# Kernel tuning notes

Hardware: AMD Instinct MI355X
Metric: run time of the kernel (lower is better)

## Reference

```python
import jax, jax.numpy as jnp
import numpy as np


def setup_inputs() -> dict:
    key = jax.random.key(0)
    k1, k2 = jax.random.split(key)
    B, N, C = 128, 200000, 100
    values = jax.random.normal(k1, (B, N), dtype=jnp.float32)
    labels = jax.random.randint(k2, (N,), 0, C, dtype=jnp.int64)
    return {"values": values, "labels": labels, "num_classes": C}


def reference(values, labels, num_classes):
    # Stratified (label-grouped) max pooling:
    # values: [B, N], labels: [N] in [0, num_classes)
    # output: [B, num_classes], out[b, c] = max over columns j with labels[j] == c
    # segment_max reduces over the leading axis, so operate on values.T [N, B].
    pooled = jax.ops.segment_max(
        values.T, labels, num_segments=num_classes, indices_are_sorted=False
    )  # [C, B]
    return pooled.T  # [B, C]
```

## Files before the change

kernel.cpp:

```cpp
#include <hip/hip_runtime.h>
#include <hip/hip_bf16.h>


#define TPB   256
#define ROWS  8
#define CACC  128

#define ENC_NEG_INF 0x007FFFFFu

__device__ __forceinline__ unsigned enc(float f) {
    unsigned u = __float_as_uint(f);
    return (u & 0x80000000u) ? ~u : (u | 0x80000000u);
}
__device__ __forceinline__ float dec(unsigned u) {
    unsigned b = (u & 0x80000000u) ? (u & 0x7FFFFFFFu) : ~u;
    return __uint_as_float(b);
}


__global__ __launch_bounds__(TPB) void strat_part(
    const float* __restrict__ values, const int* __restrict__ labels,
    unsigned* __restrict__ part, int B, int N, int C, int S, int T) {
    __shared__ unsigned acc[ROWS * CACC];

    const int tid  = threadIdx.x;
    const int bx   = blockIdx.x;
    const int row0 = blockIdx.y * ROWS;
    const int rmax = min(ROWS, B - row0);

    for (int i = tid; i < ROWS * CACC; i += TPB) acc[i] = ENC_NEG_INF;
    __syncthreads();

    for (int t = bx; t < T; t += S) {
        const int base = t * 1024 + tid * 4;
        if (t * 1024 + 1024 <= N) {
            const int4 L = *(const int4*)(labels + base);
            if (rmax == ROWS) {
                float4 v[ROWS];
#pragma unroll
                for (int r = 0; r < ROWS; ++r)
                    v[r] = *(const float4*)(values + (size_t)(row0 + r) * N + base);
#pragma unroll
                for (int r = 0; r < ROWS; ++r) {
                    unsigned* a = acc + r * CACC;
                    atomicMax(&a[L.x], enc(v[r].x));
                    atomicMax(&a[L.y], enc(v[r].y));
                    atomicMax(&a[L.z], enc(v[r].z));
                    atomicMax(&a[L.w], enc(v[r].w));
                }
            } else {
                for (int r = 0; r < rmax; ++r) {
                    float4 v = *(const float4*)(values + (size_t)(row0 + r) * N + base);
                    unsigned* a = acc + r * CACC;
                    atomicMax(&a[L.x], enc(v.x));
                    atomicMax(&a[L.y], enc(v.y));
                    atomicMax(&a[L.z], enc(v.z));
                    atomicMax(&a[L.w], enc(v.w));
                }
            }
        } else {
#pragma unroll
            for (int e = 0; e < 4; ++e) {
                const int j = base + e;
                if (j < N) {
                    const int c = labels[j];
                    for (int r = 0; r < rmax; ++r)
                        atomicMax(&acc[r * CACC + c],
                                  enc(values[(size_t)(row0 + r) * N + j]));
                }
            }
        }
    }

    __syncthreads();

    unsigned* dst = part + (size_t)bx * B * C;
    for (int i = tid; i < rmax * C; i += TPB) {
        const int r = i / C, c = i - r * C;
        dst[(size_t)(row0 + r) * C + c] = acc[r * CACC + c];
    }
}

__global__ __launch_bounds__(TPB) void strat_reduce(
    const unsigned* __restrict__ part, float* __restrict__ out, int BC, int S) {
    const int i = blockIdx.x * TPB + threadIdx.x;
    if (i >= BC) return;
    unsigned m = ENC_NEG_INF;
    for (int s = 0; s < S; ++s) m = max(m, part[(size_t)s * BC + i]);
    out[i] = dec(m);
}


#define FCPAD 257

__global__ __launch_bounds__(TPB) void strat_init(unsigned* __restrict__ out_enc, int n) {
    int i = blockIdx.x * TPB + threadIdx.x;
    if (i < n) out_enc[i] = ENC_NEG_INF;
}

__global__ __launch_bounds__(TPB) void strat_main_atomic(
    const float* __restrict__ values, const int* __restrict__ labels,
    unsigned* __restrict__ out_enc, int B, int N, int C, int T) {
    __shared__ unsigned acc[ROWS * FCPAD];
    const int tid  = threadIdx.x;
    const int row0 = blockIdx.y * ROWS;
    const int rmax = min(ROWS, B - row0);

    for (int i = tid; i < ROWS * FCPAD; i += TPB) acc[i] = ENC_NEG_INF;
    __syncthreads();

    const int t = blockIdx.x;
#pragma unroll
    for (int e = 0; e < 4; ++e) {
        const int j = t * 1024 + tid * 4 + e;
        if (j < N) {
            const int c = labels[j];
            for (int r = 0; r < rmax; ++r)
                atomicMax(&acc[r * FCPAD + c],
                          enc(values[(size_t)(row0 + r) * N + j]));
        }
    }
    __syncthreads();
    for (int i = tid; i < rmax * C; i += TPB) {
        const int r = i / C, c = i - r * C;
        atomicMax(&out_enc[(size_t)(row0 + r) * C + c], acc[r * FCPAD + c]);
    }
}

__global__ __launch_bounds__(TPB) void strat_decode(unsigned* __restrict__ buf, int n) {
    int i = blockIdx.x * TPB + threadIdx.x;
    if (i < n) {
        float f = dec(buf[i]);
        ((float*)buf)[i] = f;
    }
}


extern "C" void kernel_launch(void* const* d_in, const int* in_sizes, int n_in,
                              void* d_out, int out_size, void* d_ws, size_t ws_size,
                              hipStream_t stream) {
    const float* values = (const float*)d_in[0];
    const int*   labels = (const int*)d_in[1];
    const int N  = in_sizes[1];
    const int B  = in_sizes[0] / N;
    const int C  = out_size / B;
    const int BC = B * C;
    const int T  = (N + 1023) / 1024;
    const int RG = (B + ROWS - 1) / ROWS;

    int S = 98;
    const size_t per_split = (size_t)BC * sizeof(unsigned);
    if (per_split > 0 && (size_t)S * per_split > ws_size)
        S = (int)(ws_size / per_split);
    if (S > T) S = T;

    const bool main_ok = (S >= 1) && (C <= CACC) && (N % 4 == 0);

    if (main_ok) {
        unsigned* part = (unsigned*)d_ws;
        dim3 grid(S, RG);
        strat_part<<<grid, TPB, 0, stream>>>(values, labels, part, B, N, C, S, T);
        strat_reduce<<<(BC + TPB - 1) / TPB, TPB, 0, stream>>>(
            part, (float*)d_out, BC, S);
    } else {
        unsigned* out_enc = (unsigned*)d_out;
        const int init_blocks = (out_size + TPB - 1) / TPB;
        strat_init<<<init_blocks, TPB, 0, stream>>>(out_enc, out_size);
        dim3 grid(T, RG);
        strat_main_atomic<<<grid, TPB, 0, stream>>>(values, labels, out_enc, B, N, C, T);
        strat_decode<<<init_blocks, TPB, 0, stream>>>(out_enc, out_size);
    }
}
```

Baseline: 176.6 us.

## Replace LDS atomic max with single-wave transposed tiles and lane-per-row accumulators

The partial kernel now runs one 64-lane wave per block. Each wave stages a 64-column by 64-row tile in shared memory, and each lane owns one batch row, so per-class max updates become plain read-modify-write with no atomics or float encoding. The class label is broadcast with readlane. The reduction works directly on float partials laid out per row group and split. The tile is filled with strided column loads (each lane reads down a column of rows), which are poorly coalesced compared with the earlier float4 row loads. The accumulator takes 32KB of shared memory per block, which may limit occupancy.

```diff
diff --git a/kernel.cpp b/kernel.cpp
--- a/kernel.cpp
+++ b/kernel.cpp
@@ -2,10 +2,86 @@
 #include <hip/hip_bf16.h>
 
 
+#define WTPB 64
+#define JT   64
+#define TPAD 65
+#define CCAP 128
+#define NEGINF (-__builtin_huge_valf())
+
+__global__ __launch_bounds__(WTPB) void strat_tpose(
+    const float* __restrict__ values, const int* __restrict__ labels,
+    float* __restrict__ part, int B, int N, int C, int S, int T) {
+    __shared__ float tile[JT * TPAD];
+    __shared__ float acc[CCAP * WTPB];
+
+    const int lane = threadIdx.x;
+    const int s    = blockIdx.x;
+    const int rg   = blockIdx.y;
+    const int row0 = rg * WTPB;
+    const int rmax = min(WTPB, B - row0);
+
+    for (int i = lane; i < C * WTPB; i += WTPB) acc[i] = NEGINF;
+
+    for (int t = s; t < T; t += S) {
+        const int jc = t * JT + lane;
+        int lab = 0;
+        if (jc < N) lab = labels[jc];
+        const float* colp = values + (size_t)row0 * N + jc;
+        float* tcol = tile + lane * TPAD;
+
+        if (jc < N && rmax == WTPB) {
+#pragma unroll
+            for (int r = 0; r < WTPB; ++r)
+                tcol[r] = colp[(size_t)r * N];
+        } else {
+            for (int r = 0; r < WTPB; ++r)
+                tcol[r] = (jc < N && r < rmax) ? colp[(size_t)r * N] : NEGINF;
+        }
+
+#pragma unroll
+        for (int j = 0; j < JT; ++j) {
+            const int   c = __builtin_amdgcn_readlane(lab, j);
+            const float v = tile[j * TPAD + lane];
+            float* a = acc + c * WTPB + lane;
+            const float o = *a;
+            *a = fmaxf(o, v);
+        }
+    }
+
+    float* dst = part + ((size_t)rg * S + s) * ((size_t)C * WTPB);
+    for (int i = lane; i < C * WTPB; i += WTPB) dst[i] = acc[i];
+}
+
+__global__ __launch_bounds__(256) void strat_reduce2(
+    const float* __restrict__ part, float* __restrict__ out,
+    int B, int C, int S, int RG) {
+    const int PC = C * WTPB;
+    const int i  = blockIdx.x * 256 + threadIdx.x;
+    if (i >= RG * PC) return;
+    const int rg  = i / PC;
+    const int rem = i - rg * PC;
+    const int c   = rem >> 6;
+    const int l   = rem & 63;
+    const int b   = rg * WTPB + l;
+    if (b >= B) return;
+
+    const float* p = part + (size_t)rg * S * PC + rem;
+    float m0 = NEGINF, m1 = NEGINF, m2 = NEGINF, m3 = NEGINF;
+    int s = 0;
+    for (; s + 4 <= S; s += 4) {
+        m0 = fmaxf(m0, p[(size_t)(s + 0) * PC]);
+        m1 = fmaxf(m1, p[(size_t)(s + 1) * PC]);
+        m2 = fmaxf(m2, p[(size_t)(s + 2) * PC]);
+        m3 = fmaxf(m3, p[(size_t)(s + 3) * PC]);
+    }
+    for (; s < S; ++s) m0 = fmaxf(m0, p[(size_t)s * PC]);
+    out[b * C + c] = fmaxf(fmaxf(m0, m1), fmaxf(m2, m3));
+}
+
+
 #define TPB   256
 #define ROWS  8
-#define CACC  128
-
+#define FCPAD 257
 #define ENC_NEG_INF 0x007FFFFFu
 
 __device__ __forceinline__ unsigned enc(float f) {
@@ -16,82 +92,6 @@
     unsigned b = (u & 0x80000000u) ? (u & 0x7FFFFFFFu) : ~u;
     return __uint_as_float(b);
 }
-
-
-__global__ __launch_bounds__(TPB) void strat_part(
-    const float* __restrict__ values, const int* __restrict__ labels,
-    unsigned* __restrict__ part, int B, int N, int C, int S, int T) {
-    __shared__ unsigned acc[ROWS * CACC];
-
-    const int tid  = threadIdx.x;
-    const int bx   = blockIdx.x;
-    const int row0 = blockIdx.y * ROWS;
-    const int rmax = min(ROWS, B - row0);
-
-    for (int i = tid; i < ROWS * CACC; i += TPB) acc[i] = ENC_NEG_INF;
-    __syncthreads();
-
-    for (int t = bx; t < T; t += S) {
-        const int base = t * 1024 + tid * 4;
-        if (t * 1024 + 1024 <= N) {
-            const int4 L = *(const int4*)(labels + base);
-            if (rmax == ROWS) {
-                float4 v[ROWS];
-#pragma unroll
-                for (int r = 0; r < ROWS; ++r)
-                    v[r] = *(const float4*)(values + (size_t)(row0 + r) * N + base);
-#pragma unroll
-                for (int r = 0; r < ROWS; ++r) {
-                    unsigned* a = acc + r * CACC;
-                    atomicMax(&a[L.x], enc(v[r].x));
-                    atomicMax(&a[L.y], enc(v[r].y));
-                    atomicMax(&a[L.z], enc(v[r].z));
-                    atomicMax(&a[L.w], enc(v[r].w));
-                }
-            } else {
-                for (int r = 0; r < rmax; ++r) {
-                    float4 v = *(const float4*)(values + (size_t)(row0 + r) * N + base);
-                    unsigned* a = acc + r * CACC;
-                    atomicMax(&a[L.x], enc(v.x));
-                    atomicMax(&a[L.y], enc(v.y));
-                    atomicMax(&a[L.z], enc(v.z));
-                    atomicMax(&a[L.w], enc(v.w));
-                }
-            }
-        } else {
-#pragma unroll
-            for (int e = 0; e < 4; ++e) {
-                const int j = base + e;
-                if (j < N) {
-                    const int c = labels[j];
-                    for (int r = 0; r < rmax; ++r)
-                        atomicMax(&acc[r * CACC + c],
-                                  enc(values[(size_t)(row0 + r) * N + j]));
-                }
-            }
-        }
-    }
-
-    __syncthreads();
-
-    unsigned* dst = part + (size_t)bx * B * C;
-    for (int i = tid; i < rmax * C; i += TPB) {
-        const int r = i / C, c = i - r * C;
-        dst[(size_t)(row0 + r) * C + c] = acc[r * CACC + c];
-    }
-}
-
-__global__ __launch_bounds__(TPB) void strat_reduce(
-    const unsigned* __restrict__ part, float* __restrict__ out, int BC, int S) {
-    const int i = blockIdx.x * TPB + threadIdx.x;
-    if (i >= BC) return;
-    unsigned m = ENC_NEG_INF;
-    for (int s = 0; s < S; ++s) m = max(m, part[(size_t)s * BC + i]);
-    out[i] = dec(m);
-}
-
-
-#define FCPAD 257
 
 __global__ __launch_bounds__(TPB) void strat_init(unsigned* __restrict__ out_enc, int n) {
     int i = blockIdx.x * TPB + threadIdx.x;
@@ -144,30 +144,34 @@
     const int N  = in_sizes[1];
     const int B  = in_sizes[0] / N;
     const int C  = out_size / B;
-    const int BC = B * C;
-    const int T  = (N + 1023) / 1024;
-    const int RG = (B + ROWS - 1) / ROWS;
+    const int T  = (N + JT - 1) / JT;
+    const int RG = (B + WTPB - 1) / WTPB;
 
-    int S = 98;
-    const size_t per_split = (size_t)BC * sizeof(unsigned);
-    if (per_split > 0 && (size_t)S * per_split > ws_size)
-        S = (int)(ws_size / per_split);
+    int S = 768 / (RG > 0 ? RG : 1);
+    if (S < 1) S = 1;
     if (S > T) S = T;
+    size_t need = (size_t)RG * S * C * WTPB * sizeof(float);
+    while (S > 1 && need > ws_size) {
+        S >>= 1;
+        need = (size_t)RG * S * C * WTPB * sizeof(float);
+    }
 
-    const bool main_ok = (S >= 1) && (C <= CACC) && (N % 4 == 0);
+    const bool main_ok = (C <= CCAP) && (need <= ws_size) && (S >= 1);
 
     if (main_ok) {
-        unsigned* part = (unsigned*)d_ws;
+        float* part = (float*)d_ws;
         dim3 grid(S, RG);
-        strat_part<<<grid, TPB, 0, stream>>>(values, labels, part, B, N, C, S, T);
-        strat_reduce<<<(BC + TPB - 1) / TPB, TPB, 0, stream>>>(
-            part, (float*)d_out, BC, S);
+        strat_tpose<<<grid, WTPB, 0, stream>>>(values, labels, part, B, N, C, S, T);
+        const int outs = RG * C * WTPB;
+        strat_reduce2<<<(outs + 255) / 256, 256, 0, stream>>>(
+            part, (float*)d_out, B, C, S, RG);
     } else {
         unsigned* out_enc = (unsigned*)d_out;
         const int init_blocks = (out_size + TPB - 1) / TPB;
         strat_init<<<init_blocks, TPB, 0, stream>>>(out_enc, out_size);
-        dim3 grid(T, RG);
-        strat_main_atomic<<<grid, TPB, 0, stream>>>(values, labels, out_enc, B, N, C, T);
+        dim3 grid((N + 1023) / 1024, (B + ROWS - 1) / ROWS);
+        strat_main_atomic<<<grid, TPB, 0, stream>>>(values, labels, out_enc, B, N, C,
+                                                    (N + 1023) / 1024);
         strat_decode<<<init_blocks, TPB, 0, stream>>>(out_enc, out_size);
     }
 }
```

After: 201.3 us. +14.0%, slower.

## Restructure segment max into per-row span streaming with byte labels

Applied to the files above, without the earlier changes.

Labels are first compacted to 8-bit in the workspace. The main kernel then assigns each block a single row and a contiguous span of columns (16 spans per row), streams values with nontemporal vector loads, and spreads atomics over four padded LDS copies, one per group of 16 lanes within each wavefront, to cut contention. The final reduction loop is unrolled by four, and a branchless float encoding replaces the conditional one. The extra label-conversion launch and the loss of label reuse across eight rows trade against better load coalescing and fewer LDS conflicts.

```diff
diff --git a/kernel.cpp b/kernel.cpp
--- a/kernel.cpp
+++ b/kernel.cpp
@@ -2,96 +2,95 @@
 #include <hip/hip_bf16.h>
 
 
-#define TPB   256
-#define ROWS  8
-#define CACC  128
-
+#define TPBS 256
+#define SMAX 16
 #define ENC_NEG_INF 0x007FFFFFu
 
-__device__ __forceinline__ unsigned enc(float f) {
-    unsigned u = __float_as_uint(f);
-    return (u & 0x80000000u) ? ~u : (u | 0x80000000u);
+typedef float f4 __attribute__((ext_vector_type(4)));
+
+__device__ __forceinline__ unsigned enc32(unsigned u) {
+    return u ^ ((unsigned)(((int)u) >> 31) | 0x80000000u);
 }
-__device__ __forceinline__ float dec(unsigned u) {
-    unsigned b = (u & 0x80000000u) ? (u & 0x7FFFFFFFu) : ~u;
+__device__ __forceinline__ float dec32(unsigned u) {
+    unsigned b = u ^ (~(unsigned)(((int)u) >> 31) | 0x80000000u);
     return __uint_as_float(b);
 }
 
+__global__ __launch_bounds__(TPBS) void strat_lab8(
+    const int* __restrict__ labels, unsigned char* __restrict__ l8, int N) {
+    int i = blockIdx.x * TPBS + threadIdx.x;
+    if (i < N) l8[i] = (unsigned char)labels[i];
+}
 
-__global__ __launch_bounds__(TPB) void strat_part(
-    const float* __restrict__ values, const int* __restrict__ labels,
-    unsigned* __restrict__ part, int B, int N, int C, int S, int T) {
-    __shared__ unsigned acc[ROWS * CACC];
+__global__ __launch_bounds__(TPBS) void strat_stream(
+    const float* __restrict__ values, const unsigned char* __restrict__ l8,
+    unsigned* __restrict__ part, int B, int N, int C, int S, int SPAN, int CPAD) {
+    extern __shared__ unsigned acc[];
 
-    const int tid  = threadIdx.x;
-    const int bx   = blockIdx.x;
-    const int row0 = blockIdx.y * ROWS;
-    const int rmax = min(ROWS, B - row0);
+    const int tid = threadIdx.x;
+    const int blk = blockIdx.x;
+    const int s   = blk % S;
+    const int b   = blk / S;
 
-    for (int i = tid; i < ROWS * CACC; i += TPB) acc[i] = ENC_NEG_INF;
+    for (int i = tid; i < 4 * CPAD; i += TPBS) acc[i] = ENC_NEG_INF;
     __syncthreads();
 
-    for (int t = bx; t < T; t += S) {
-        const int base = t * 1024 + tid * 4;
-        if (t * 1024 + 1024 <= N) {
-            const int4 L = *(const int4*)(labels + base);
-            if (rmax == ROWS) {
-                float4 v[ROWS];
-#pragma unroll
-                for (int r = 0; r < ROWS; ++r)
-                    v[r] = *(const float4*)(values + (size_t)(row0 + r) * N + base);
-#pragma unroll
-                for (int r = 0; r < ROWS; ++r) {
-                    unsigned* a = acc + r * CACC;
-                    atomicMax(&a[L.x], enc(v[r].x));
-                    atomicMax(&a[L.y], enc(v[r].y));
-                    atomicMax(&a[L.z], enc(v[r].z));
-                    atomicMax(&a[L.w], enc(v[r].w));
-                }
-            } else {
-                for (int r = 0; r < rmax; ++r) {
-                    float4 v = *(const float4*)(values + (size_t)(row0 + r) * N + base);
-                    unsigned* a = acc + r * CACC;
-                    atomicMax(&a[L.x], enc(v.x));
-                    atomicMax(&a[L.y], enc(v.y));
-                    atomicMax(&a[L.z], enc(v.z));
-                    atomicMax(&a[L.w], enc(v.w));
-                }
-            }
-        } else {
-#pragma unroll
-            for (int e = 0; e < 4; ++e) {
-                const int j = base + e;
-                if (j < N) {
-                    const int c = labels[j];
-                    for (int r = 0; r < rmax; ++r)
-                        atomicMax(&acc[r * CACC + c],
-                                  enc(values[(size_t)(row0 + r) * N + j]));
-                }
-            }
+    const int off0 = s * SPAN;
+    const int len  = min(SPAN, N - off0);
+    if (len > 0) {
+        unsigned* qacc = acc + ((tid & 63) >> 4) * CPAD;
+        const f4* vp = (const f4*)(values + (size_t)b * N + off0);
+        const uchar4* lp = (const uchar4*)(l8 + off0);
+        const int nv = len >> 2;
+
+        for (int i = tid; i < nv; i += TPBS) {
+            f4 v = __builtin_nontemporal_load(vp + i);
+            uchar4 L = lp[i];
+            atomicMax(&qacc[L.x], enc32(__float_as_uint(v.x)));
+            atomicMax(&qacc[L.y], enc32(__float_as_uint(v.y)));
+            atomicMax(&qacc[L.z], enc32(__float_as_uint(v.z)));
+            atomicMax(&qacc[L.w], enc32(__float_as_uint(v.w)));
+        }
+        for (int i = (nv << 2) + tid; i < len; i += TPBS) {
+            atomicMax(&qacc[l8[off0 + i]],
+                      enc32(__float_as_uint(values[(size_t)b * N + off0 + i])));
         }
     }
-
     __syncthreads();
 
-    unsigned* dst = part + (size_t)bx * B * C;
-    for (int i = tid; i < rmax * C; i += TPB) {
-        const int r = i / C, c = i - r * C;
-        dst[(size_t)(row0 + r) * C + c] = acc[r * CACC + c];
+    unsigned* dst = part + (size_t)s * B * C + (size_t)b * C;
+    for (int c = tid; c < C; c += TPBS) {
+        unsigned m = max(max(acc[c], acc[CPAD + c]),
+                         max(acc[2 * CPAD + c], acc[3 * CPAD + c]));
+        dst[c] = m;
     }
 }
 
-__global__ __launch_bounds__(TPB) void strat_reduce(
+__global__ __launch_bounds__(TPBS) void strat_red(
     const unsigned* __restrict__ part, float* __restrict__ out, int BC, int S) {
-    const int i = blockIdx.x * TPB + threadIdx.x;
+    const int i = blockIdx.x * TPBS + threadIdx.x;
     if (i >= BC) return;
-    unsigned m = ENC_NEG_INF;
-    for (int s = 0; s < S; ++s) m = max(m, part[(size_t)s * BC + i]);
-    out[i] = dec(m);
+    const unsigned* p = part + i;
+    unsigned m0 = ENC_NEG_INF, m1 = ENC_NEG_INF, m2 = ENC_NEG_INF, m3 = ENC_NEG_INF;
+    int s = 0;
+    for (; s + 4 <= S; s += 4) {
+        m0 = max(m0, p[(size_t)(s + 0) * BC]);
+        m1 = max(m1, p[(size_t)(s + 1) * BC]);
+        m2 = max(m2, p[(size_t)(s + 2) * BC]);
+        m3 = max(m3, p[(size_t)(s + 3) * BC]);
+    }
+    for (; s < S; ++s) m0 = max(m0, p[(size_t)s * BC]);
+    out[i] = dec32(max(max(m0, m1), max(m2, m3)));
 }
 
 
+#define TPB   256
+#define ROWS  8
 #define FCPAD 257
+
+__device__ __forceinline__ unsigned encf(float f) {
+    return enc32(__float_as_uint(f));
+}
 
 __global__ __launch_bounds__(TPB) void strat_init(unsigned* __restrict__ out_enc, int n) {
     int i = blockIdx.x * TPB + threadIdx.x;
@@ -117,7 +116,7 @@
             const int c = labels[j];
             for (int r = 0; r < rmax; ++r)
                 atomicMax(&acc[r * FCPAD + c],
-                          enc(values[(size_t)(row0 + r) * N + j]));
+                          encf(values[(size_t)(row0 + r) * N + j]));
         }
     }
     __syncthreads();
@@ -130,7 +129,7 @@
 __global__ __launch_bounds__(TPB) void strat_decode(unsigned* __restrict__ buf, int n) {
     int i = blockIdx.x * TPB + threadIdx.x;
     if (i < n) {
-        float f = dec(buf[i]);
+        float f = dec32(buf[i]);
         ((float*)buf)[i] = f;
     }
 }
@@ -145,29 +144,36 @@
     const int B  = in_sizes[0] / N;
     const int C  = out_size / B;
     const int BC = B * C;
-    const int T  = (N + 1023) / 1024;
-    const int RG = (B + ROWS - 1) / ROWS;
 
-    int S = 98;
-    const size_t per_split = (size_t)BC * sizeof(unsigned);
-    if (per_split > 0 && (size_t)S * per_split > ws_size)
-        S = (int)(ws_size / per_split);
-    if (S > T) S = T;
+    const int S    = SMAX;
+    const int SPAN = (((N + S - 1) / S) + 3) & ~3;
+    const int CPAD = ((C + 31) / 32) * 32 + 1;
 
-    const bool main_ok = (S >= 1) && (C <= CACC) && (N % 4 == 0);
+    const size_t part_off   = ((size_t)N + 255) & ~(size_t)255;
+    const size_t part_bytes = (size_t)S * BC * sizeof(unsigned);
+    const size_t lds        = (size_t)4 * CPAD * sizeof(unsigned);
+
+    const bool main_ok = (C <= 128) && (part_off + part_bytes <= ws_size) &&
+                         ((size_t)S * SPAN >= (size_t)N);
 
     if (main_ok) {
-        unsigned* part = (unsigned*)d_ws;
-        dim3 grid(S, RG);
-        strat_part<<<grid, TPB, 0, stream>>>(values, labels, part, B, N, C, S, T);
-        strat_reduce<<<(BC + TPB - 1) / TPB, TPB, 0, stream>>>(
+        unsigned char* l8   = (unsigned char*)d_ws;
+        unsigned*      part = (unsigned*)((char*)d_ws + part_off);
+
+        strat_lab8<<<(N + TPBS - 1) / TPBS, TPBS, 0, stream>>>(labels, l8, N);
+
+        strat_stream<<<S * B, TPBS, lds, stream>>>(
+            values, l8, part, B, N, C, S, SPAN, CPAD);
+
+        strat_red<<<(BC + TPBS - 1) / TPBS, TPBS, 0, stream>>>(
             part, (float*)d_out, BC, S);
     } else {
         unsigned* out_enc = (unsigned*)d_out;
         const int init_blocks = (out_size + TPB - 1) / TPB;
         strat_init<<<init_blocks, TPB, 0, stream>>>(out_enc, out_size);
-        dim3 grid(T, RG);
-        strat_main_atomic<<<grid, TPB, 0, stream>>>(values, labels, out_enc, B, N, C, T);
+        dim3 grid((N + 1023) / 1024, (B + ROWS - 1) / ROWS);
+        strat_main_atomic<<<grid, TPB, 0, stream>>>(values, labels, out_enc, B, N, C,
+                                                    (N + 1023) / 1024);
         strat_decode<<<init_blocks, TPB, 0, stream>>>(out_enc, out_size);
     }
 }
```

Result: faster. 146.2 us (-17.2%).
